# Performance work log

Hardware: AMD Instinct MI355X
Metric: run time of the kernel (lower is better)

## Reference

```python
import jax, jax.numpy as jnp
import numpy as np

N = 100000   # nodes
E = 800000   # edges
F_IN = 16
H = 64       # hidden_dim
L = 4        # num_layers
CD = 8       # contrastive_dim
BN_EPS = 1e-5


def setup_inputs() -> dict:
    key = jax.random.key(0)
    ks = jax.random.split(key, 20)
    s = 0.05
    return {
        "x": jax.random.normal(ks[0], (N, F_IN), jnp.float32),
        "edge_index": jax.random.randint(ks[1], (2, E), 0, N, jnp.int64),
        "batch": jnp.zeros((N,), jnp.int64),
        "enc_w1": jax.random.normal(ks[2], (F_IN, H), jnp.float32) * s,
        "enc_b1": jnp.zeros((H,), jnp.float32),
        "enc_w2": jax.random.normal(ks[3], (H, H), jnp.float32) * s,
        "enc_b2": jnp.zeros((H,), jnp.float32),
        "conv_w": jax.random.normal(ks[4], (L, 2 * H, H), jnp.float32) * s,
        "conv_b": jnp.zeros((L, H), jnp.float32),
        "bn_gamma": jnp.ones((L, H), jnp.float32),
        "bn_beta": jnp.zeros((L, H), jnp.float32),
        "out_w1": jax.random.normal(ks[5], (H, 64), jnp.float32) * s,
        "out_b1": jnp.zeros((64,), jnp.float32),
        "out_w2": jax.random.normal(ks[6], (64, 32), jnp.float32) * s,
        "out_b2": jnp.zeros((32,), jnp.float32),
        "out_w3": jax.random.normal(ks[7], (32, CD), jnp.float32) * s,
        "out_b3": jnp.zeros((CD,), jnp.float32),
    }


def _forward(x, edge_index, enc_w1, enc_b1, enc_w2, enc_b2,
             conv_w, conv_b, bn_gamma, bn_beta,
             out_w1, out_b1, out_w2, out_b2, out_w3, out_b3):
    row, col = edge_index[0], edge_index[1]
    # lc_encode: Linear+ELU, Linear+ELU
    h = jax.nn.elu(x @ enc_w1 + enc_b1)
    feats = jax.nn.elu(h @ enc_w2 + enc_b2)  # (N, H)

    ones = jnp.ones((E, 1), feats.dtype)
    counts = jnp.clip(jax.ops.segment_sum(ones, row, num_segments=N), 1.0)  # (N,1)
    bn_scale = 1.0 / jnp.sqrt(1.0 + BN_EPS)  # eval-mode BN: running_mean=0, running_var=1

    for i in range(L):
        xc = feats[row]               # gather centers (E, H)
        xn = feats[col]               # gather neighbors (E, H)
        ef = jnp.concatenate([xc, xn - xc], axis=-1)      # (E, 2H)
        e = jax.nn.elu(ef @ conv_w[i] + conv_b[i])        # Linear + ELU
        e = (e * bn_scale) * bn_gamma[i] + bn_beta[i]     # BatchNorm (eval); Dropout is identity
        agg = jax.ops.segment_sum(e, row, num_segments=N) / counts
        feats = agg + feats  # residual in Net.forward

    # output head (Dropout identity in eval)
    o = jax.nn.elu(feats @ out_w1 + out_b1)
    o = jax.nn.elu(o @ out_w2 + out_b2)
    return o @ out_w3 + out_b3  # (N, CD)


def reference(x, edge_index, batch, enc_w1, enc_b1, enc_w2, enc_b2,
              conv_w, conv_b, bn_gamma, bn_beta,
              out_w1, out_b1, out_w2, out_b2, out_w3, out_b3):
    out = _forward(x, edge_index, enc_w1, enc_b1, enc_w2, enc_b2,
                   conv_w, conv_b, bn_gamma, bn_beta,
                   out_w1, out_b1, out_w2, out_b2, out_w3, out_b3)
    return (out, batch)
```

## Files before the change

kernel.cpp:

```cpp
#include <hip/hip_runtime.h>

#define NN 100000
#define NE 800000
#define FIN 16
#define H 64
#define NL 4
#define CDIM 8
#define NT 1563
#define NABF 1563
#define NGB 6250
#define NGF 12500
#define ROWS_PER_OWN 12500
#define ECHUNK 2048
#define NCHUNK ((NE + ECHUNK - 1) / ECHUNK)
#define NSC (NCHUNK * 8)
#define CAP 32
#define HOT 8
#define SPILL (CAP - HOT)

typedef __attribute__((ext_vector_type(8))) short bf16x8;
typedef __attribute__((ext_vector_type(4))) float f32x4;

__device__ __forceinline__ float elu(float x) { return x > 0.f ? x : __expf(x) - 1.f; }
__device__ __forceinline__ float4 elu4(float4 v) {
    return make_float4(elu(v.x), elu(v.y), elu(v.z), elu(v.w));
}

__device__ __forceinline__ unsigned short f2bf(float x) {
    union { float f; unsigned int u; } v; v.f = x;
    unsigned int r = v.u + 0x7fffu + ((v.u >> 16) & 1u);
    return (unsigned short)(r >> 16);
}
__device__ __forceinline__ float u2f(unsigned int u) {
    union { unsigned int u; float f; } v; v.u = u;
    return v.f;
}

__global__ __launch_bounds__(256) void k_enc(const float* __restrict__ x,
                                             const float* __restrict__ w1,
                                             const float* __restrict__ b1,
                                             const float* __restrict__ w2,
                                             const float* __restrict__ b2,
                                             float* __restrict__ feats,
                                             int* __restrict__ cnt,
                                             const float* __restrict__ convw,
                                             unsigned short* __restrict__ WT) {
    int tid = threadIdx.x;
    if (blockIdx.x >= NT) {
        int t = (blockIdx.x - NT) * 256 + tid;
        int i = t >> 11;
        int rem = t & 2047;
        int j = rem >> 4;
        int kg = rem & 15;
        const float* W = convw + (size_t)i * 2 * H * H;
        float v[4];
#pragma unroll
        for (int q = 0; q < 4; q++) {
            int k = kg * 4 + q;
            if (j < 64) v[q] = W[k * 64 + j] - W[(64 + k) * 64 + j];
            else        v[q] = W[(64 + k) * 64 + (j - 64)];
        }
        ushort4 p;
        p.x = f2bf(v[0]); p.y = f2bf(v[1]); p.z = f2bf(v[2]); p.w = f2bf(v[3]);
        *(ushort4*)&WT[(size_t)i * 8192 + j * 64 + kg * 4] = p;
        return;
    }
    __shared__ __align__(16) float xs[64 * 16];
    __shared__ __align__(16) float w1s[16 * 64];
    __shared__ __align__(16) float ws[64 * 64];
    __shared__ __align__(16) float fs[64 * 68];
    int base = blockIdx.x * 64;
    {
        int gid = blockIdx.x * 256 + tid;
        if (gid < NN) cnt[gid] = 0;
    }
    {
        size_t ei = (size_t)base * FIN + tid * 4;
        size_t emax = (size_t)NN * FIN - 4;
        if (ei > emax) ei = emax;
        *(float4*)&xs[tid * 4] = *(const float4*)&x[ei];
    }
    ((float4*)w1s)[tid] = ((const float4*)w1)[tid];
#pragma unroll
    for (int r = 0; r < 4; r++) ((float4*)ws)[tid + 256 * r] = ((const float4*)w2)[tid + 256 * r];
    __syncthreads();

    int wave = tid >> 6, j = tid & 63;
    float bb1 = b1[j];
    for (int i = 0; i < 16; i++) {
        int nl = i * 4 + wave;
        float acc = bb1;
#pragma unroll
        for (int k = 0; k < FIN; k++) acc += xs[nl * FIN + k] * w1s[k * 64 + j];
        fs[nl * 68 + j] = elu(acc);
    }
    __syncthreads();

    int cg = tid & 15, ng = tid >> 4;
    int c0 = cg * 4;
    float4 bb = ((const float4*)b2)[cg];
    float4 acc[4];
    acc[0] = bb; acc[1] = bb; acc[2] = bb; acc[3] = bb;
#pragma unroll 2
    for (int kq = 0; kq < 16; kq++) {
        int k0 = kq * 4;
        float4 w0 = *(const float4*)&ws[(k0 + 0) * 64 + c0];
        float4 w1v = *(const float4*)&ws[(k0 + 1) * 64 + c0];
        float4 w2v = *(const float4*)&ws[(k0 + 2) * 64 + c0];
        float4 w3v = *(const float4*)&ws[(k0 + 3) * 64 + c0];
#pragma unroll
        for (int m = 0; m < 4; m++) {
            float4 f = *(const float4*)&fs[(ng * 4 + m) * 68 + k0];
            acc[m].x += f.x * w0.x + f.y * w1v.x + f.z * w2v.x + f.w * w3v.x;
            acc[m].y += f.x * w0.y + f.y * w1v.y + f.z * w2v.y + f.w * w3v.y;
            acc[m].z += f.x * w0.z + f.y * w1v.z + f.z * w2v.z + f.w * w3v.z;
            acc[m].w += f.x * w0.w + f.y * w1v.w + f.z * w2v.w + f.w * w3v.w;
        }
    }
#pragma unroll
    for (int m = 0; m < 4; m++) {
        int n = base + ng * 4 + m;
        if (n < NN) *(float4*)&feats[(size_t)n * 64 + c0] = elu4(acc[m]);
    }
}

__global__ __launch_bounds__(256, 8) void k_scab(const int* __restrict__ row,
                                                 const int* __restrict__ col,
                                                 int* cnt, int* __restrict__ hot,
                                                 int* __restrict__ spill,
                                                 const float* __restrict__ feats,
                                                 const unsigned short* __restrict__ WT,
                                                 const float* __restrict__ convb,
                                                 unsigned short* __restrict__ Am,
                                                 unsigned short* __restrict__ Bm) {
    int tid = threadIdx.x;
    if (blockIdx.x >= NABF) {
        int owner = blockIdx.x & 7;
        int chunk = (blockIdx.x - NABF) >> 3;
        int lo = owner * ROWS_PER_OWN, hi = lo + ROWS_PER_OWN;
        int base = chunk * ECHUNK;
        int end = base + ECHUNK; if (end > NE) end = NE;
        for (int e = base + tid; e < end; e += 256) {
            int r = row[e];
            if (r >= lo && r < hi) {
                int p = atomicAdd(&cnt[r], 1);
                if (p < HOT) hot[(size_t)r * HOT + p] = col[e];
                else if (p < CAP) spill[(size_t)r * SPILL + (p - HOT)] = col[e];
            }
        }
        return;
    }
    int bid = blockIdx.x;
    int wave = tid >> 6, lane = tid & 63;
    int lr = lane & 15, lk = lane >> 4;
    int nb = bid * 64 + wave * 16;
    int n = nb + lr;
    int nc = n < NN ? n : NN - 1;

    bf16x8 ff0, ff1;
    {
        float4 f0 = *(const float4*)&feats[(size_t)nc * 64 + lk * 8];
        float4 f1 = *(const float4*)&feats[(size_t)nc * 64 + lk * 8 + 4];
        float4 f2 = *(const float4*)&feats[(size_t)nc * 64 + 32 + lk * 8];
        float4 f3 = *(const float4*)&feats[(size_t)nc * 64 + 32 + lk * 8 + 4];
        ff0[0] = (short)f2bf(f0.x); ff0[1] = (short)f2bf(f0.y);
        ff0[2] = (short)f2bf(f0.z); ff0[3] = (short)f2bf(f0.w);
        ff0[4] = (short)f2bf(f1.x); ff0[5] = (short)f2bf(f1.y);
        ff0[6] = (short)f2bf(f1.z); ff0[7] = (short)f2bf(f1.w);
        ff1[0] = (short)f2bf(f2.x); ff1[1] = (short)f2bf(f2.y);
        ff1[2] = (short)f2bf(f2.z); ff1[3] = (short)f2bf(f2.w);
        ff1[4] = (short)f2bf(f3.x); ff1[5] = (short)f2bf(f3.y);
        ff1[6] = (short)f2bf(f3.z); ff1[7] = (short)f2bf(f3.w);
    }
#pragma unroll 1
    for (int ct = 0; ct < 8; ct++) {
        bf16x8 w0 = *(const bf16x8*)&WT[(ct * 16 + lr) * 64 + lk * 8];
        bf16x8 w1 = *(const bf16x8*)&WT[(ct * 16 + lr) * 64 + 32 + lk * 8];
        f32x4 acc;
        if (ct < 4) {
            float4 bq = *(const float4*)&convb[ct * 16 + lk * 4];
            acc[0] = bq.x; acc[1] = bq.y; acc[2] = bq.z; acc[3] = bq.w;
        } else {
            acc = (f32x4)(0.0f);
        }
        acc = __builtin_amdgcn_mfma_f32_16x16x32_bf16(w0, ff0, acc, 0, 0, 0);
        acc = __builtin_amdgcn_mfma_f32_16x16x32_bf16(w1, ff1, acc, 0, 0, 0);
        if (n < NN) {
            unsigned short* dst = (ct < 4) ? Am : Bm;
            int wc = (ct & 3) * 16 + lk * 4;
            ushort4 p;
            p.x = f2bf(acc[0]); p.y = f2bf(acc[1]);
            p.z = f2bf(acc[2]); p.w = f2bf(acc[3]);
            *(ushort4*)&dst[(size_t)n * 64 + wc] = p;
        }
    }
}

__global__ __launch_bounds__(256) void k_gab(const unsigned short* __restrict__ Brd,
                                             unsigned short* __restrict__ Am,
                                             unsigned short* __restrict__ Bwr,
                                             const int* __restrict__ cnt,
                                             const int* __restrict__ hot,
                                             const int* __restrict__ spill,
                                             const float* __restrict__ gamma,
                                             const float* __restrict__ beta,
                                             float* __restrict__ feats,
                                             const unsigned short* __restrict__ WT,
                                             const float* __restrict__ convb) {
    __shared__ __align__(16) unsigned short nlds[16 * 72];
    int tid = threadIdx.x;
    int wave = tid >> 6, lane = tid & 63;
    int half = lane >> 5, l = lane & 31;
    int g = l >> 3;
    int cq = l & 7, c0 = cq * 8;
    int nb16 = blockIdx.x * 16;

    const float bs = 0.99999500003749968750f;
    float4 gm0 = *(const float4*)&gamma[c0];
    float4 gm1 = *(const float4*)&gamma[c0 + 4];
    float4 bt0 = *(const float4*)&beta[c0];
    float4 bt1 = *(const float4*)&beta[c0 + 4];

#pragma unroll
    for (int t = 0; t < 2; t++) {
        int j = t * 8 + wave * 2 + half;
        int n = nb16 + j;
        int deg = cnt[n];
        if (deg > CAP) deg = CAP;
        int mycol = (l < HOT) ? hot[(size_t)n * HOT + l]
                              : spill[(size_t)n * SPILL + (l - HOT)];
        uint4 rawA = *(const uint4*)&Am[(size_t)n * H + c0];
        float4 a0 = make_float4(u2f(rawA.x << 16), u2f(rawA.x & 0xffff0000u),
                                u2f(rawA.y << 16), u2f(rawA.y & 0xffff0000u));
        float4 a1 = make_float4(u2f(rawA.z << 16), u2f(rawA.z & 0xffff0000u),
                                u2f(rawA.w << 16), u2f(rawA.w & 0xffff0000u));
        float4 f0, f1;
        if (g == 0) {
            f0 = *(const float4*)&feats[(size_t)n * H + c0];
            f1 = *(const float4*)&feats[(size_t)n * H + c0 + 4];
        }
        float4 acc0 = make_float4(0.f, 0.f, 0.f, 0.f);
        float4 acc1 = make_float4(0.f, 0.f, 0.f, 0.f);
        for (int p0 = 0; p0 < deg; p0 += 4) {
            int p = p0 + g;
            bool valid = p < deg;
            int pc = valid ? p : (deg - 1);
            int c = __shfl(mycol, (half << 5) + pc);
            uint4 raw = *(const uint4*)&Brd[(size_t)c * H + c0];
            float4 b0 = make_float4(u2f(raw.x << 16), u2f(raw.x & 0xffff0000u),
                                    u2f(raw.y << 16), u2f(raw.y & 0xffff0000u));
            float4 b1 = make_float4(u2f(raw.z << 16), u2f(raw.z & 0xffff0000u),
                                    u2f(raw.w << 16), u2f(raw.w & 0xffff0000u));
            float4 v0 = elu4(make_float4(a0.x + b0.x, a0.y + b0.y, a0.z + b0.z, a0.w + b0.w));
            float4 v1 = elu4(make_float4(a1.x + b1.x, a1.y + b1.y, a1.z + b1.z, a1.w + b1.w));
            if (valid) {
                acc0.x += v0.x; acc0.y += v0.y; acc0.z += v0.z; acc0.w += v0.w;
                acc1.x += v1.x; acc1.y += v1.y; acc1.z += v1.z; acc1.w += v1.w;
            }
        }
#pragma unroll
        for (int d = 8; d < 32; d <<= 1) {
            acc0.x += __shfl_xor(acc0.x, d); acc0.y += __shfl_xor(acc0.y, d);
            acc0.z += __shfl_xor(acc0.z, d); acc0.w += __shfl_xor(acc0.w, d);
            acc1.x += __shfl_xor(acc1.x, d); acc1.y += __shfl_xor(acc1.y, d);
            acc1.z += __shfl_xor(acc1.z, d); acc1.w += __shfl_xor(acc1.w, d);
        }
        if (g == 0) {
            if (deg > 0) {
                float inv = bs / (float)deg;
                f0.x += acc0.x * gm0.x * inv + bt0.x;
                f0.y += acc0.y * gm0.y * inv + bt0.y;
                f0.z += acc0.z * gm0.z * inv + bt0.z;
                f0.w += acc0.w * gm0.w * inv + bt0.w;
                f1.x += acc1.x * gm1.x * inv + bt1.x;
                f1.y += acc1.y * gm1.y * inv + bt1.y;
                f1.z += acc1.z * gm1.z * inv + bt1.z;
                f1.w += acc1.w * gm1.w * inv + bt1.w;
                *(float4*)&feats[(size_t)n * H + c0] = f0;
                *(float4*)&feats[(size_t)n * H + c0 + 4] = f1;
            }
            ushort4 pa, pb;
            pa.x = f2bf(f0.x); pa.y = f2bf(f0.y); pa.z = f2bf(f0.z); pa.w = f2bf(f0.w);
            pb.x = f2bf(f1.x); pb.y = f2bf(f1.y); pb.z = f2bf(f1.z); pb.w = f2bf(f1.w);
            *(ushort4*)&nlds[j * 72 + cq * 8] = pa;
            *(ushort4*)&nlds[j * 72 + cq * 8 + 4] = pb;
        }
    }
    __syncthreads();

    {
        int lr = lane & 15, lk = lane >> 4;
        bf16x8 ff[2];
#pragma unroll
        for (int kt = 0; kt < 2; kt++)
            ff[kt] = *(const bf16x8*)&nlds[lr * 72 + kt * 32 + lk * 8];
#pragma unroll
        for (int ctl = 0; ctl < 2; ctl++) {
            int ct = wave * 2 + ctl;
            bf16x8 w0 = *(const bf16x8*)&WT[(ct * 16 + lr) * 64 + lk * 8];
            bf16x8 w1 = *(const bf16x8*)&WT[(ct * 16 + lr) * 64 + 32 + lk * 8];
            f32x4 acc;
            if (ct < 4) {
                float4 bq = *(const float4*)&convb[ct * 16 + lk * 4];
                acc[0] = bq.x; acc[1] = bq.y; acc[2] = bq.z; acc[3] = bq.w;
            } else {
                acc = (f32x4)(0.0f);
            }
            acc = __builtin_amdgcn_mfma_f32_16x16x32_bf16(w0, ff[0], acc, 0, 0, 0);
            acc = __builtin_amdgcn_mfma_f32_16x16x32_bf16(w1, ff[1], acc, 0, 0, 0);
            int n = nb16 + lr;
            unsigned short* dst = (ct < 4) ? Am : Bwr;
            int wc = (ct & 3) * 16 + lk * 4;
            ushort4 p;
            p.x = f2bf(acc[0]); p.y = f2bf(acc[1]);
            p.z = f2bf(acc[2]); p.w = f2bf(acc[3]);
            *(ushort4*)&dst[(size_t)n * 64 + wc] = p;
        }
    }
}

__global__ __launch_bounds__(256) void k_gather(const unsigned short* __restrict__ Am,
                                                const unsigned short* __restrict__ Bm,
                                                const int* __restrict__ cnt,
                                                const int* __restrict__ hot,
                                                const int* __restrict__ spill,
                                                const float* __restrict__ gamma,
                                                const float* __restrict__ beta,
                                                float* __restrict__ feats) {
    int tid = threadIdx.x;
    int wave = tid >> 6, lane = tid & 63;
    int half = lane >> 5, l = lane & 31;
    int n = blockIdx.x * 8 + wave * 2 + half;
    int g = l >> 3;
    int cq = l & 7, c0 = cq * 8;
    int deg = cnt[n];
    if (deg > CAP) deg = CAP;
    int mycol = (l < HOT) ? hot[(size_t)n * HOT + l]
                          : spill[(size_t)n * SPILL + (l - HOT)];
    uint4 rawA = *(const uint4*)&Am[(size_t)n * H + c0];
    float4 a0 = make_float4(u2f(rawA.x << 16), u2f(rawA.x & 0xffff0000u),
                            u2f(rawA.y << 16), u2f(rawA.y & 0xffff0000u));
    float4 a1 = make_float4(u2f(rawA.z << 16), u2f(rawA.z & 0xffff0000u),
                            u2f(rawA.w << 16), u2f(rawA.w & 0xffff0000u));
    float4 f0, f1;
    if (g == 0) {
        f0 = *(const float4*)&feats[(size_t)n * H + c0];
        f1 = *(const float4*)&feats[(size_t)n * H + c0 + 4];
    }
    float4 acc0 = make_float4(0.f, 0.f, 0.f, 0.f);
    float4 acc1 = make_float4(0.f, 0.f, 0.f, 0.f);
    for (int p0 = 0; p0 < deg; p0 += 4) {
        int p = p0 + g;
        bool valid = p < deg;
        int pc = valid ? p : (deg - 1);
        int c = __shfl(mycol, (half << 5) + pc);
        uint4 raw = *(const uint4*)&Bm[(size_t)c * H + c0];
        float4 b0 = make_float4(u2f(raw.x << 16), u2f(raw.x & 0xffff0000u),
                                u2f(raw.y << 16), u2f(raw.y & 0xffff0000u));
        float4 b1 = make_float4(u2f(raw.z << 16), u2f(raw.z & 0xffff0000u),
                                u2f(raw.w << 16), u2f(raw.w & 0xffff0000u));
        float4 v0 = elu4(make_float4(a0.x + b0.x, a0.y + b0.y, a0.z + b0.z, a0.w + b0.w));
        float4 v1 = elu4(make_float4(a1.x + b1.x, a1.y + b1.y, a1.z + b1.z, a1.w + b1.w));
        if (valid) {
            acc0.x += v0.x; acc0.y += v0.y; acc0.z += v0.z; acc0.w += v0.w;
            acc1.x += v1.x; acc1.y += v1.y; acc1.z += v1.z; acc1.w += v1.w;
        }
    }
#pragma unroll
    for (int d = 8; d < 32; d <<= 1) {
        acc0.x += __shfl_xor(acc0.x, d); acc0.y += __shfl_xor(acc0.y, d);
        acc0.z += __shfl_xor(acc0.z, d); acc0.w += __shfl_xor(acc0.w, d);
        acc1.x += __shfl_xor(acc1.x, d); acc1.y += __shfl_xor(acc1.y, d);
        acc1.z += __shfl_xor(acc1.z, d); acc1.w += __shfl_xor(acc1.w, d);
    }
    if (g == 0 && deg > 0) {
        const float bs = 0.99999500003749968750f;
        float inv = bs / (float)deg;
        float4 gm0 = *(const float4*)&gamma[c0];
        float4 gm1 = *(const float4*)&gamma[c0 + 4];
        float4 bt0 = *(const float4*)&beta[c0];
        float4 bt1 = *(const float4*)&beta[c0 + 4];
        f0.x += acc0.x * gm0.x * inv + bt0.x;
        f0.y += acc0.y * gm0.y * inv + bt0.y;
        f0.z += acc0.z * gm0.z * inv + bt0.z;
        f0.w += acc0.w * gm0.w * inv + bt0.w;
        f1.x += acc1.x * gm1.x * inv + bt1.x;
        f1.y += acc1.y * gm1.y * inv + bt1.y;
        f1.z += acc1.z * gm1.z * inv + bt1.z;
        f1.w += acc1.w * gm1.w * inv + bt1.w;
        *(float4*)&feats[(size_t)n * H + c0] = f0;
        *(float4*)&feats[(size_t)n * H + c0 + 4] = f1;
    }
}

__global__ __launch_bounds__(256) void k_head(const float* __restrict__ feats,
                                              const float* __restrict__ w1,
                                              const float* __restrict__ b1,
                                              const float* __restrict__ w2,
                                              const float* __restrict__ b2,
                                              const float* __restrict__ w3,
                                              const float* __restrict__ b3,
                                              const int* __restrict__ batch,
                                              float* __restrict__ out,
                                              float* __restrict__ out2) {
    __shared__ __align__(16) float fs[64 * 68];
    __shared__ __align__(16) float w1s[64 * 64];
    __shared__ __align__(16) float o1s[64 * 68];
    __shared__ __align__(16) float w2s[64 * 32];
    __shared__ __align__(16) float w3s[32 * 8];
    int tid = threadIdx.x;
    int base = blockIdx.x * 64;
#pragma unroll
    for (int r = 0; r < 4; r++) {
        int idx = tid + 256 * r;
        ((float4*)w1s)[idx] = ((const float4*)w1)[idx];
        int rw = idx >> 4, cc = idx & 15;
        int n = base + rw; if (n >= NN) n = NN - 1;
        *(float4*)&fs[rw * 68 + cc * 4] = *(const float4*)&feats[(size_t)n * 64 + cc * 4];
    }
    ((float4*)w2s)[tid] = ((const float4*)w2)[tid];
    ((float4*)w2s)[tid + 256] = ((const float4*)w2)[tid + 256];
    if (tid < 64) ((float4*)w3s)[tid] = ((const float4*)w3)[tid];
    if (tid < 64) {
        int n = base + tid;
        if (n < NN) out2[n] = (float)batch[n];
    }
    __syncthreads();

    int cg = tid & 15, ng = tid >> 4;
    int c0 = cg * 4;
    {
        float4 bb = ((const float4*)b1)[cg];
        float4 acc[4];
        acc[0] = bb; acc[1] = bb; acc[2] = bb; acc[3] = bb;
#pragma unroll 2
        for (int kq = 0; kq < 16; kq++) {
            int k0 = kq * 4;
            float4 w0 = *(const float4*)&w1s[(k0 + 0) * 64 + c0];
            float4 w1v = *(const float4*)&w1s[(k0 + 1) * 64 + c0];
            float4 w2v = *(const float4*)&w1s[(k0 + 2) * 64 + c0];
            float4 w3v = *(const float4*)&w1s[(k0 + 3) * 64 + c0];
#pragma unroll
            for (int m = 0; m < 4; m++) {
                float4 f = *(const float4*)&fs[(ng * 4 + m) * 68 + k0];
                acc[m].x += f.x * w0.x + f.y * w1v.x + f.z * w2v.x + f.w * w3v.x;
                acc[m].y += f.x * w0.y + f.y * w1v.y + f.z * w2v.y + f.w * w3v.y;
                acc[m].z += f.x * w0.z + f.y * w1v.z + f.z * w2v.z + f.w * w3v.z;
                acc[m].w += f.x * w0.w + f.y * w1v.w + f.z * w2v.w + f.w * w3v.w;
            }
        }
        __syncthreads();
#pragma unroll
        for (int m = 0; m < 4; m++)
            *(float4*)&o1s[(ng * 4 + m) * 68 + c0] = elu4(acc[m]);
    }
    __syncthreads();

    float* o2s = fs;
    {
        int cg2 = tid & 7, ng2 = tid >> 3;
        int c20 = cg2 * 4;
        float4 bb = ((const float4*)b2)[cg2];
        float4 acc[2];
        acc[0] = bb; acc[1] = bb;
#pragma unroll 2
        for (int kq = 0; kq < 16; kq++) {
            int k0 = kq * 4;
            float4 w0 = *(const float4*)&w2s[(k0 + 0) * 32 + c20];
            float4 w1v = *(const float4*)&w2s[(k0 + 1) * 32 + c20];
            float4 w2v = *(const float4*)&w2s[(k0 + 2) * 32 + c20];
            float4 w3v = *(const float4*)&w2s[(k0 + 3) * 32 + c20];
#pragma unroll
            for (int m = 0; m < 2; m++) {
                float4 f = *(const float4*)&o1s[(ng2 * 2 + m) * 68 + k0];
                acc[m].x += f.x * w0.x + f.y * w1v.x + f.z * w2v.x + f.w * w3v.x;
                acc[m].y += f.x * w0.y + f.y * w1v.y + f.z * w2v.y + f.w * w3v.y;
                acc[m].z += f.x * w0.z + f.y * w1v.z + f.z * w2v.z + f.w * w3v.z;
                acc[m].w += f.x * w0.w + f.y * w1v.w + f.z * w2v.w + f.w * w3v.w;
            }
        }
#pragma unroll
        for (int m = 0; m < 2; m++)
            *(float4*)&o2s[(ng2 * 2 + m) * 40 + c20] = elu4(acc[m]);
    }
    __syncthreads();

    if (tid < 128) {
        int n3 = tid >> 1, c30 = (tid & 1) * 4;
        float4 acc = ((const float4*)b3)[tid & 1];
#pragma unroll 2
        for (int kq = 0; kq < 8; kq++) {
            int k0 = kq * 4;
            float4 w0 = *(const float4*)&w3s[(k0 + 0) * 8 + c30];
            float4 w1v = *(const float4*)&w3s[(k0 + 1) * 8 + c30];
            float4 w2v = *(const float4*)&w3s[(k0 + 2) * 8 + c30];
            float4 w3v = *(const float4*)&w3s[(k0 + 3) * 8 + c30];
            float4 f = *(const float4*)&o2s[n3 * 40 + k0];
            acc.x += f.x * w0.x + f.y * w1v.x + f.z * w2v.x + f.w * w3v.x;
            acc.y += f.x * w0.y + f.y * w1v.y + f.z * w2v.y + f.w * w3v.y;
            acc.z += f.x * w0.z + f.y * w1v.z + f.z * w2v.z + f.w * w3v.z;
            acc.w += f.x * w0.w + f.y * w1v.w + f.z * w2v.w + f.w * w3v.w;
        }
        int n = base + n3;
        if (n < NN) *(float4*)&out[(size_t)n * 8 + c30] = acc;
    }
}

extern "C" void kernel_launch(void* const* d_in, const int* in_sizes, int n_in,
                              void* d_out, int out_size, void* d_ws, size_t ws_size,
                              hipStream_t stream) {
    const float* x = (const float*)d_in[0];
    const int* edge_index = (const int*)d_in[1];
    const int* batch = (const int*)d_in[2];
    const float* enc_w1 = (const float*)d_in[3];
    const float* enc_b1 = (const float*)d_in[4];
    const float* enc_w2 = (const float*)d_in[5];
    const float* enc_b2 = (const float*)d_in[6];
    const float* conv_w = (const float*)d_in[7];
    const float* conv_b = (const float*)d_in[8];
    const float* bn_gamma = (const float*)d_in[9];
    const float* bn_beta = (const float*)d_in[10];
    const float* out_w1 = (const float*)d_in[11];
    const float* out_b1 = (const float*)d_in[12];
    const float* out_w2 = (const float*)d_in[13];
    const float* out_b2 = (const float*)d_in[14];
    const float* out_w3 = (const float*)d_in[15];
    const float* out_b3 = (const float*)d_in[16];

    const int* row = edge_index;
    const int* col = edge_index + NE;

    float* feats = (float*)d_ws;
    unsigned short* Abuf = (unsigned short*)(feats + (size_t)NN * H);
    unsigned short* Bbuf0 = Abuf + (size_t)NN * H;
    unsigned short* Bbuf1 = Bbuf0 + (size_t)NN * H;
    int* cnt = (int*)(Bbuf1 + (size_t)NN * H);
    int* hot = cnt + NN;
    int* spill = hot + (size_t)NN * HOT;
    unsigned short* WT = (unsigned short*)(spill + (size_t)NN * SPILL);

    float* out = (float*)d_out;

    k_enc<<<NT + 32, 256, 0, stream>>>(x, enc_w1, enc_b1, enc_w2, enc_b2, feats, cnt,
                                       conv_w, WT);
    k_scab<<<NABF + NSC, 256, 0, stream>>>(row, col, cnt, hot, spill,
                                           feats, WT, conv_b, Abuf, Bbuf0);

    unsigned short* Brd = Bbuf0;
    unsigned short* Bwr = Bbuf1;
    for (int i = 0; i < NL - 1; i++) {
        k_gab<<<NGB, 256, 0, stream>>>(Brd, Abuf, Bwr, cnt, hot, spill,
                                       bn_gamma + (size_t)i * H, bn_beta + (size_t)i * H,
                                       feats, WT + (size_t)(i + 1) * 8192,
                                       conv_b + (size_t)(i + 1) * H);
        unsigned short* tmp = Brd; Brd = Bwr; Bwr = tmp;
    }
    k_gather<<<NGF, 256, 0, stream>>>(Abuf, Brd, cnt, hot, spill,
                                      bn_gamma + (size_t)(NL - 1) * H,
                                      bn_beta + (size_t)(NL - 1) * H, feats);

    k_head<<<NT, 256, 0, stream>>>(feats, out_w1, out_b1, out_w2, out_b2,
                                   out_w3, out_b3, batch, out,
                                   out + (size_t)NN * CDIM);
}
```

Before: 369.6 us.

## Fuse final gather-aggregate layer with output MLP head into one kernel

Merges the last-layer neighbor gather/aggregation kernel with the three-layer output head, so each 8-node block aggregates its features into shared memory and immediately runs the MLP. This removes the final feats write/read round trip and one kernel launch. The cost is that each of the 12500 blocks now reloads about 25 KB of head weights into shared memory, and the head matmuls now use a less register-blocked scalar scheme over only 8 nodes.

After: 388.1 us. 1.05x slower.

```diff
diff --git a/kernel.cpp b/kernel.cpp
--- a/kernel.cpp
+++ b/kernel.cpp
@@ -9,7 +9,7 @@
 #define NT 1563
 #define NABF 1563
 #define NGB 6250
-#define NGF 12500
+#define NGH 12500
 #define ROWS_PER_OWN 12500
 #define ECHUNK 2048
 #define NCHUNK ((NE + ECHUNK - 1) / ECHUNK)
@@ -319,190 +319,140 @@
     }
 }
 
-__global__ __launch_bounds__(256) void k_gather(const unsigned short* __restrict__ Am,
-                                                const unsigned short* __restrict__ Bm,
-                                                const int* __restrict__ cnt,
-                                                const int* __restrict__ hot,
-                                                const int* __restrict__ spill,
-                                                const float* __restrict__ gamma,
-                                                const float* __restrict__ beta,
-                                                float* __restrict__ feats) {
-    int tid = threadIdx.x;
-    int wave = tid >> 6, lane = tid & 63;
-    int half = lane >> 5, l = lane & 31;
-    int n = blockIdx.x * 8 + wave * 2 + half;
-    int g = l >> 3;
-    int cq = l & 7, c0 = cq * 8;
-    int deg = cnt[n];
-    if (deg > CAP) deg = CAP;
-    int mycol = (l < HOT) ? hot[(size_t)n * HOT + l]
-                          : spill[(size_t)n * SPILL + (l - HOT)];
-    uint4 rawA = *(const uint4*)&Am[(size_t)n * H + c0];
-    float4 a0 = make_float4(u2f(rawA.x << 16), u2f(rawA.x & 0xffff0000u),
-                            u2f(rawA.y << 16), u2f(rawA.y & 0xffff0000u));
-    float4 a1 = make_float4(u2f(rawA.z << 16), u2f(rawA.z & 0xffff0000u),
-                            u2f(rawA.w << 16), u2f(rawA.w & 0xffff0000u));
-    float4 f0, f1;
-    if (g == 0) {
-        f0 = *(const float4*)&feats[(size_t)n * H + c0];
-        f1 = *(const float4*)&feats[(size_t)n * H + c0 + 4];
-    }
-    float4 acc0 = make_float4(0.f, 0.f, 0.f, 0.f);
-    float4 acc1 = make_float4(0.f, 0.f, 0.f, 0.f);
-    for (int p0 = 0; p0 < deg; p0 += 4) {
-        int p = p0 + g;
-        bool valid = p < deg;
-        int pc = valid ? p : (deg - 1);
-        int c = __shfl(mycol, (half << 5) + pc);
-        uint4 raw = *(const uint4*)&Bm[(size_t)c * H + c0];
-        float4 b0 = make_float4(u2f(raw.x << 16), u2f(raw.x & 0xffff0000u),
-                                u2f(raw.y << 16), u2f(raw.y & 0xffff0000u));
-        float4 b1 = make_float4(u2f(raw.z << 16), u2f(raw.z & 0xffff0000u),
-                                u2f(raw.w << 16), u2f(raw.w & 0xffff0000u));
-        float4 v0 = elu4(make_float4(a0.x + b0.x, a0.y + b0.y, a0.z + b0.z, a0.w + b0.w));
-        float4 v1 = elu4(make_float4(a1.x + b1.x, a1.y + b1.y, a1.z + b1.z, a1.w + b1.w));
-        if (valid) {
-            acc0.x += v0.x; acc0.y += v0.y; acc0.z += v0.z; acc0.w += v0.w;
-            acc1.x += v1.x; acc1.y += v1.y; acc1.z += v1.z; acc1.w += v1.w;
-        }
-    }
-#pragma unroll
-    for (int d = 8; d < 32; d <<= 1) {
-        acc0.x += __shfl_xor(acc0.x, d); acc0.y += __shfl_xor(acc0.y, d);
-        acc0.z += __shfl_xor(acc0.z, d); acc0.w += __shfl_xor(acc0.w, d);
-        acc1.x += __shfl_xor(acc1.x, d); acc1.y += __shfl_xor(acc1.y, d);
-        acc1.z += __shfl_xor(acc1.z, d); acc1.w += __shfl_xor(acc1.w, d);
-    }
-    if (g == 0 && deg > 0) {
-        const float bs = 0.99999500003749968750f;
-        float inv = bs / (float)deg;
-        float4 gm0 = *(const float4*)&gamma[c0];
-        float4 gm1 = *(const float4*)&gamma[c0 + 4];
-        float4 bt0 = *(const float4*)&beta[c0];
-        float4 bt1 = *(const float4*)&beta[c0 + 4];
-        f0.x += acc0.x * gm0.x * inv + bt0.x;
-        f0.y += acc0.y * gm0.y * inv + bt0.y;
-        f0.z += acc0.z * gm0.z * inv + bt0.z;
-        f0.w += acc0.w * gm0.w * inv + bt0.w;
-        f1.x += acc1.x * gm1.x * inv + bt1.x;
-        f1.y += acc1.y * gm1.y * inv + bt1.y;
-        f1.z += acc1.z * gm1.z * inv + bt1.z;
-        f1.w += acc1.w * gm1.w * inv + bt1.w;
-        *(float4*)&feats[(size_t)n * H + c0] = f0;
-        *(float4*)&feats[(size_t)n * H + c0 + 4] = f1;
-    }
-}
-
-__global__ __launch_bounds__(256) void k_head(const float* __restrict__ feats,
-                                              const float* __restrict__ w1,
-                                              const float* __restrict__ b1,
-                                              const float* __restrict__ w2,
-                                              const float* __restrict__ b2,
-                                              const float* __restrict__ w3,
-                                              const float* __restrict__ b3,
-                                              const int* __restrict__ batch,
-                                              float* __restrict__ out,
-                                              float* __restrict__ out2) {
-    __shared__ __align__(16) float fs[64 * 68];
+__global__ __launch_bounds__(256) void k_ghead(const unsigned short* __restrict__ Am,
+                                               const unsigned short* __restrict__ Bm,
+                                               const int* __restrict__ cnt,
+                                               const int* __restrict__ hot,
+                                               const int* __restrict__ spill,
+                                               const float* __restrict__ gamma,
+                                               const float* __restrict__ beta,
+                                               const float* __restrict__ feats,
+                                               const float* __restrict__ w1,
+                                               const float* __restrict__ b1,
+                                               const float* __restrict__ w2,
+                                               const float* __restrict__ b2,
+                                               const float* __restrict__ w3,
+                                               const float* __restrict__ b3,
+                                               const int* __restrict__ batch,
+                                               float* __restrict__ out,
+                                               float* __restrict__ out2) {
     __shared__ __align__(16) float w1s[64 * 64];
-    __shared__ __align__(16) float o1s[64 * 68];
     __shared__ __align__(16) float w2s[64 * 32];
     __shared__ __align__(16) float w3s[32 * 8];
+    __shared__ __align__(16) float fs[8 * 68];
+    __shared__ __align__(16) float o1s[8 * 68];
     int tid = threadIdx.x;
-    int base = blockIdx.x * 64;
-#pragma unroll
-    for (int r = 0; r < 4; r++) {
-        int idx = tid + 256 * r;
-        ((float4*)w1s)[idx] = ((const float4*)w1)[idx];
-        int rw = idx >> 4, cc = idx & 15;
-        int n = base + rw; if (n >= NN) n = NN - 1;
-        *(float4*)&fs[rw * 68 + cc * 4] = *(const float4*)&feats[(size_t)n * 64 + cc * 4];
-    }
+    int base8 = blockIdx.x * 8;
+
+#pragma unroll
+    for (int r = 0; r < 4; r++) ((float4*)w1s)[tid + 256 * r] = ((const float4*)w1)[tid + 256 * r];
     ((float4*)w2s)[tid] = ((const float4*)w2)[tid];
     ((float4*)w2s)[tid + 256] = ((const float4*)w2)[tid + 256];
     if (tid < 64) ((float4*)w3s)[tid] = ((const float4*)w3)[tid];
+    if (tid < 8) out2[base8 + tid] = (float)batch[base8 + tid];
+
+    {
+        int wave = tid >> 6, lane = tid & 63;
+        int half = lane >> 5, l = lane & 31;
+        int j8 = wave * 2 + half;
+        int n = base8 + j8;
+        int g = l >> 3;
+        int cq = l & 7, c0 = cq * 8;
+        int deg = cnt[n];
+        if (deg > CAP) deg = CAP;
+        int mycol = (l < HOT) ? hot[(size_t)n * HOT + l]
+                              : spill[(size_t)n * SPILL + (l - HOT)];
+        uint4 rawA = *(const uint4*)&Am[(size_t)n * H + c0];
+        float4 a0 = make_float4(u2f(rawA.x << 16), u2f(rawA.x & 0xffff0000u),
+                                u2f(rawA.y << 16), u2f(rawA.y & 0xffff0000u));
+        float4 a1 = make_float4(u2f(rawA.z << 16), u2f(rawA.z & 0xffff0000u),
+                                u2f(rawA.w << 16), u2f(rawA.w & 0xffff0000u));
+        float4 f0, f1;
+        if (g == 0) {
+            f0 = *(const float4*)&feats[(size_t)n * H + c0];
+            f1 = *(const float4*)&feats[(size_t)n * H + c0 + 4];
+        }
+        float4 acc0 = make_float4(0.f, 0.f, 0.f, 0.f);
+        float4 acc1 = make_float4(0.f, 0.f, 0.f, 0.f);
+        for (int p0 = 0; p0 < deg; p0 += 4) {
+            int p = p0 + g;
+            bool valid = p < deg;
+            int pc = valid ? p : (deg - 1);
+            int c = __shfl(mycol, (half << 5) + pc);
+            uint4 raw = *(const uint4*)&Bm[(size_t)c * H + c0];
+            float4 b0 = make_float4(u2f(raw.x << 16), u2f(raw.x & 0xffff0000u),
+                                    u2f(raw.y << 16), u2f(raw.y & 0xffff0000u));
+            float4 b1 = make_float4(u2f(raw.z << 16), u2f(raw.z & 0xffff0000u),
+                                    u2f(raw.w << 16), u2f(raw.w & 0xffff0000u));
+            float4 v0 = elu4(make_float4(a0.x + b0.x, a0.y + b0.y, a0.z + b0.z, a0.w + b0.w));
+            float4 v1 = elu4(make_float4(a1.x + b1.x, a1.y + b1.y, a1.z + b1.z, a1.w + b1.w));
+            if (valid) {
+                acc0.x += v0.x; acc0.y += v0.y; acc0.z += v0.z; acc0.w += v0.w;
+                acc1.x += v1.x; acc1.y += v1.y; acc1.z += v1.z; acc1.w += v1.w;
+            }
+        }
+#pragma unroll
+        for (int d = 8; d < 32; d <<= 1) {
+            acc0.x += __shfl_xor(acc0.x, d); acc0.y += __shfl_xor(acc0.y, d);
+            acc0.z += __shfl_xor(acc0.z, d); acc0.w += __shfl_xor(acc0.w, d);
+            acc1.x += __shfl_xor(acc1.x, d); acc1.y += __shfl_xor(acc1.y, d);
+            acc1.z += __shfl_xor(acc1.z, d); acc1.w += __shfl_xor(acc1.w, d);
+        }
+        if (g == 0) {
+            if (deg > 0) {
+                const float bs = 0.99999500003749968750f;
+                float inv = bs / (float)deg;
+                float4 gm0 = *(const float4*)&gamma[c0];
+                float4 gm1 = *(const float4*)&gamma[c0 + 4];
+                float4 bt0 = *(const float4*)&beta[c0];
+                float4 bt1 = *(const float4*)&beta[c0 + 4];
+                f0.x += acc0.x * gm0.x * inv + bt0.x;
+                f0.y += acc0.y * gm0.y * inv + bt0.y;
+                f0.z += acc0.z * gm0.z * inv + bt0.z;
+                f0.w += acc0.w * gm0.w * inv + bt0.w;
+                f1.x += acc1.x * gm1.x * inv + bt1.x;
+                f1.y += acc1.y * gm1.y * inv + bt1.y;
+                f1.z += acc1.z * gm1.z * inv + bt1.z;
+                f1.w += acc1.w * gm1.w * inv + bt1.w;
+            }
+            *(float4*)&fs[j8 * 68 + c0] = f0;
+            *(float4*)&fs[j8 * 68 + c0 + 4] = f1;
+        }
+    }
+    __syncthreads();
+
+    {
+        int j = tid & 63, w = tid >> 6;
+        float a0 = b1[j], a1 = a0;
+#pragma unroll 4
+        for (int k = 0; k < 64; k++) {
+            float wv = w1s[k * 64 + j];
+            a0 += fs[(2 * w) * 68 + k] * wv;
+            a1 += fs[(2 * w + 1) * 68 + k] * wv;
+        }
+        o1s[(2 * w) * 68 + j] = elu(a0);
+        o1s[(2 * w + 1) * 68 + j] = elu(a1);
+    }
+    __syncthreads();
+
+    float* o2s = fs;
+    {
+        int node = tid >> 5, j2 = tid & 31;
+        float a = b2[j2];
+#pragma unroll 4
+        for (int k = 0; k < 64; k++) a += o1s[node * 68 + k] * w2s[k * 32 + j2];
+        float r = elu(a);
+        __syncthreads();
+        o2s[node * 40 + j2] = r;
+    }
+    __syncthreads();
+
     if (tid < 64) {
-        int n = base + tid;
-        if (n < NN) out2[n] = (float)batch[n];
-    }
-    __syncthreads();
-
-    int cg = tid & 15, ng = tid >> 4;
-    int c0 = cg * 4;
-    {
-        float4 bb = ((const float4*)b1)[cg];
-        float4 acc[4];
-        acc[0] = bb; acc[1] = bb; acc[2] = bb; acc[3] = bb;
-#pragma unroll 2
-        for (int kq = 0; kq < 16; kq++) {
-            int k0 = kq * 4;
-            float4 w0 = *(const float4*)&w1s[(k0 + 0) * 64 + c0];
-            float4 w1v = *(const float4*)&w1s[(k0 + 1) * 64 + c0];
-            float4 w2v = *(const float4*)&w1s[(k0 + 2) * 64 + c0];
-            float4 w3v = *(const float4*)&w1s[(k0 + 3) * 64 + c0];
-#pragma unroll
-            for (int m = 0; m < 4; m++) {
-                float4 f = *(const float4*)&fs[(ng * 4 + m) * 68 + k0];
-                acc[m].x += f.x * w0.x + f.y * w1v.x + f.z * w2v.x + f.w * w3v.x;
-                acc[m].y += f.x * w0.y + f.y * w1v.y + f.z * w2v.y + f.w * w3v.y;
-                acc[m].z += f.x * w0.z + f.y * w1v.z + f.z * w2v.z + f.w * w3v.z;
-                acc[m].w += f.x * w0.w + f.y * w1v.w + f.z * w2v.w + f.w * w3v.w;
-            }
-        }
-        __syncthreads();
-#pragma unroll
-        for (int m = 0; m < 4; m++)
-            *(float4*)&o1s[(ng * 4 + m) * 68 + c0] = elu4(acc[m]);
-    }
-    __syncthreads();
-
-    float* o2s = fs;
-    {
-        int cg2 = tid & 7, ng2 = tid >> 3;
-        int c20 = cg2 * 4;
-        float4 bb = ((const float4*)b2)[cg2];
-        float4 acc[2];
-        acc[0] = bb; acc[1] = bb;
-#pragma unroll 2
-        for (int kq = 0; kq < 16; kq++) {
-            int k0 = kq * 4;
-            float4 w0 = *(const float4*)&w2s[(k0 + 0) * 32 + c20];
-            float4 w1v = *(const float4*)&w2s[(k0 + 1) * 32 + c20];
-            float4 w2v = *(const float4*)&w2s[(k0 + 2) * 32 + c20];
-            float4 w3v = *(const float4*)&w2s[(k0 + 3) * 32 + c20];
-#pragma unroll
-            for (int m = 0; m < 2; m++) {
-                float4 f = *(const float4*)&o1s[(ng2 * 2 + m) * 68 + k0];
-                acc[m].x += f.x * w0.x + f.y * w1v.x + f.z * w2v.x + f.w * w3v.x;
-                acc[m].y += f.x * w0.y + f.y * w1v.y + f.z * w2v.y + f.w * w3v.y;
-                acc[m].z += f.x * w0.z + f.y * w1v.z + f.z * w2v.z + f.w * w3v.z;
-                acc[m].w += f.x * w0.w + f.y * w1v.w + f.z * w2v.w + f.w * w3v.w;
-            }
-        }
-#pragma unroll
-        for (int m = 0; m < 2; m++)
-            *(float4*)&o2s[(ng2 * 2 + m) * 40 + c20] = elu4(acc[m]);
-    }
-    __syncthreads();
-
-    if (tid < 128) {
-        int n3 = tid >> 1, c30 = (tid & 1) * 4;
-        float4 acc = ((const float4*)b3)[tid & 1];
-#pragma unroll 2
-        for (int kq = 0; kq < 8; kq++) {
-            int k0 = kq * 4;
-            float4 w0 = *(const float4*)&w3s[(k0 + 0) * 8 + c30];
-            float4 w1v = *(const float4*)&w3s[(k0 + 1) * 8 + c30];
-            float4 w2v = *(const float4*)&w3s[(k0 + 2) * 8 + c30];
-            float4 w3v = *(const float4*)&w3s[(k0 + 3) * 8 + c30];
-            float4 f = *(const float4*)&o2s[n3 * 40 + k0];
-            acc.x += f.x * w0.x + f.y * w1v.x + f.z * w2v.x + f.w * w3v.x;
-            acc.y += f.x * w0.y + f.y * w1v.y + f.z * w2v.y + f.w * w3v.y;
-            acc.z += f.x * w0.z + f.y * w1v.z + f.z * w2v.z + f.w * w3v.z;
-            acc.w += f.x * w0.w + f.y * w1v.w + f.z * w2v.w + f.w * w3v.w;
-        }
-        int n = base + n3;
-        if (n < NN) *(float4*)&out[(size_t)n * 8 + c30] = acc;
+        int node = tid >> 3, c3 = tid & 7;
+        float a = b3[c3];
+#pragma unroll 4
+        for (int k = 0; k < 32; k++) a += o2s[node * 40 + k] * w3s[k * 8 + c3];
+        out[(size_t)(base8 + node) * 8 + c3] = a;
     }
 }
 
@@ -555,11 +505,9 @@
                                        conv_b + (size_t)(i + 1) * H);
         unsigned short* tmp = Brd; Brd = Bwr; Bwr = tmp;
     }
-    k_gather<<<NGF, 256, 0, stream>>>(Abuf, Brd, cnt, hot, spill,
-                                      bn_gamma + (size_t)(NL - 1) * H,
-                                      bn_beta + (size_t)(NL - 1) * H, feats);
-
-    k_head<<<NT, 256, 0, stream>>>(feats, out_w1, out_b1, out_w2, out_b2,
-                                   out_w3, out_b3, batch, out,
-                                   out + (size_t)NN * CDIM);
-}
+    k_ghead<<<NGH, 256, 0, stream>>>(Abuf, Brd, cnt, hot, spill,
+                                     bn_gamma + (size_t)(NL - 1) * H,
+                                     bn_beta + (size_t)(NL - 1) * H, feats,
+                                     out_w1, out_b1, out_w2, out_b2, out_w3, out_b3,
+                                     batch, out, out + (size_t)NN * CDIM);
+}
```

## Fuse layer kernels into persistent cooperative kernel with grid sync and atomic tile tickets

Applied to the files above, without the earlier changes.

The three per-layer gather/MFMA kernels and the final gather kernel are replaced by one persistent cooperative kernel. It loops over the layers with grid.sync between them and takes 16-node tiles from an atomic ticket counter that k_enc zeroes each call. The aim is to remove kernel launch gaps and tail effects between layers. In exchange it adds per-tile atomic and barrier overhead, caps residency at the occupancy limit, and grid-wide barriers can cost as much as launch boundaries.

Result: slower. 1.424 ms (+285.3%).

```diff
diff --git a/kernel.cpp b/kernel.cpp
--- a/kernel.cpp
+++ b/kernel.cpp
@@ -1,4 +1,7 @@
 #include <hip/hip_runtime.h>
+#include <hip/hip_cooperative_groups.h>
+
+namespace cg = cooperative_groups;
 
 #define NN 100000
 #define NE 800000
@@ -44,7 +47,8 @@
                                              float* __restrict__ feats,
                                              int* __restrict__ cnt,
                                              const float* __restrict__ convw,
-                                             unsigned short* __restrict__ WT) {
+                                             unsigned short* __restrict__ WT,
+                                             int* __restrict__ tickets) {
     int tid = threadIdx.x;
     if (blockIdx.x >= NT) {
         int t = (blockIdx.x - NT) * 256 + tid;
@@ -74,6 +78,7 @@
         int gid = blockIdx.x * 256 + tid;
         if (gid < NN) cnt[gid] = 0;
     }
+    if (blockIdx.x == 0 && tid < 4) tickets[tid] = 0;
     {
         size_t ei = (size_t)base * FIN + tid * 4;
         size_t emax = (size_t)NN * FIN - 4;
@@ -96,9 +101,9 @@
     }
     __syncthreads();
 
-    int cg = tid & 15, ng = tid >> 4;
-    int c0 = cg * 4;
-    float4 bb = ((const float4*)b2)[cg];
+    int cg_ = tid & 15, ng = tid >> 4;
+    int c0 = cg_ * 4;
+    float4 bb = ((const float4*)b2)[cg_];
     float4 acc[4];
     acc[0] = bb; acc[1] = bb; acc[2] = bb; acc[3] = bb;
 #pragma unroll 2
@@ -196,24 +201,25 @@
     }
 }
 
-__global__ __launch_bounds__(256) void k_gab(const unsigned short* __restrict__ Brd,
-                                             unsigned short* __restrict__ Am,
-                                             unsigned short* __restrict__ Bwr,
-                                             const int* __restrict__ cnt,
-                                             const int* __restrict__ hot,
-                                             const int* __restrict__ spill,
-                                             const float* __restrict__ gamma,
-                                             const float* __restrict__ beta,
-                                             float* __restrict__ feats,
-                                             const unsigned short* __restrict__ WT,
-                                             const float* __restrict__ convb) {
-    __shared__ __align__(16) unsigned short nlds[16 * 72];
+__device__ __forceinline__ void gab_tile(int tile,
+                                         const unsigned short* __restrict__ Brd,
+                                         unsigned short* __restrict__ Am,
+                                         unsigned short* __restrict__ Bwr,
+                                         const int* __restrict__ cnt,
+                                         const int* __restrict__ hot,
+                                         const int* __restrict__ spill,
+                                         const float* __restrict__ gamma,
+                                         const float* __restrict__ beta,
+                                         float* __restrict__ feats,
+                                         const unsigned short* __restrict__ WT,
+                                         const float* __restrict__ convb,
+                                         unsigned short* nlds) {
     int tid = threadIdx.x;
     int wave = tid >> 6, lane = tid & 63;
     int half = lane >> 5, l = lane & 31;
     int g = l >> 3;
     int cq = l & 7, c0 = cq * 8;
-    int nb16 = blockIdx.x * 16;
+    int nb16 = tile * 16;
 
     const float bs = 0.99999500003749968750f;
     float4 gm0 = *(const float4*)&gamma[c0];
@@ -319,18 +325,19 @@
     }
 }
 
-__global__ __launch_bounds__(256) void k_gather(const unsigned short* __restrict__ Am,
-                                                const unsigned short* __restrict__ Bm,
-                                                const int* __restrict__ cnt,
-                                                const int* __restrict__ hot,
-                                                const int* __restrict__ spill,
-                                                const float* __restrict__ gamma,
-                                                const float* __restrict__ beta,
-                                                float* __restrict__ feats) {
+__device__ __forceinline__ void g3_tile(int tile,
+                                        const unsigned short* __restrict__ Am,
+                                        const unsigned short* __restrict__ Bm,
+                                        const int* __restrict__ cnt,
+                                        const int* __restrict__ hot,
+                                        const int* __restrict__ spill,
+                                        const float* __restrict__ gamma,
+                                        const float* __restrict__ beta,
+                                        float* __restrict__ feats) {
     int tid = threadIdx.x;
     int wave = tid >> 6, lane = tid & 63;
     int half = lane >> 5, l = lane & 31;
-    int n = blockIdx.x * 8 + wave * 2 + half;
+    int n = tile * 8 + wave * 2 + half;
     int g = l >> 3;
     int cq = l & 7, c0 = cq * 8;
     int deg = cnt[n];
@@ -393,6 +400,81 @@
     }
 }
 
+__global__ __launch_bounds__(256) void k_gab(const unsigned short* __restrict__ Brd,
+                                             unsigned short* __restrict__ Am,
+                                             unsigned short* __restrict__ Bwr,
+                                             const int* __restrict__ cnt,
+                                             const int* __restrict__ hot,
+                                             const int* __restrict__ spill,
+                                             const float* __restrict__ gamma,
+                                             const float* __restrict__ beta,
+                                             float* __restrict__ feats,
+                                             const unsigned short* __restrict__ WT,
+                                             const float* __restrict__ convb) {
+    __shared__ __align__(16) unsigned short nlds[16 * 72];
+    gab_tile(blockIdx.x, Brd, Am, Bwr, cnt, hot, spill, gamma, beta, feats, WT, convb, nlds);
+}
+
+__global__ __launch_bounds__(256) void k_gather(const unsigned short* __restrict__ Am,
+                                                const unsigned short* __restrict__ Bm,
+                                                const int* __restrict__ cnt,
+                                                const int* __restrict__ hot,
+                                                const int* __restrict__ spill,
+                                                const float* __restrict__ gamma,
+                                                const float* __restrict__ beta,
+                                                float* __restrict__ feats) {
+    g3_tile(blockIdx.x, Am, Bm, cnt, hot, spill, gamma, beta, feats);
+}
+
+__global__ __launch_bounds__(256, 8) void k_mega(unsigned short* Am,
+                                                 unsigned short* Bbuf0,
+                                                 unsigned short* Bbuf1,
+                                                 const int* cnt,
+                                                 const int* hot,
+                                                 const int* spill,
+                                                 const float* bn_gamma,
+                                                 const float* bn_beta,
+                                                 float* feats,
+                                                 const unsigned short* WT,
+                                                 const float* convb,
+                                                 int* tickets) {
+    cg::grid_group grid = cg::this_grid();
+    __shared__ __align__(16) unsigned short nlds[16 * 72];
+    __shared__ int s_tile;
+    int tid = threadIdx.x;
+
+    for (int layer = 0; layer < 3; layer++) {
+        const unsigned short* Brd = (layer & 1) ? Bbuf1 : Bbuf0;
+        unsigned short* Bwr = (layer & 1) ? Bbuf0 : Bbuf1;
+        const float* gamma = bn_gamma + (size_t)layer * H;
+        const float* beta = bn_beta + (size_t)layer * H;
+        const unsigned short* WTl = WT + (size_t)(layer + 1) * 8192;
+        const float* cb = convb + (size_t)(layer + 1) * H;
+        while (true) {
+            __syncthreads();
+            if (tid == 0) s_tile = atomicAdd(&tickets[layer], 1);
+            __syncthreads();
+            int t = s_tile;
+            if (t >= NGB) break;
+            gab_tile(t, Brd, Am, Bwr, cnt, hot, spill, gamma, beta, feats, WTl, cb, nlds);
+        }
+        __threadfence();
+        grid.sync();
+    }
+    {
+        const float* gamma = bn_gamma + (size_t)3 * H;
+        const float* beta = bn_beta + (size_t)3 * H;
+        while (true) {
+            __syncthreads();
+            if (tid == 0) s_tile = atomicAdd(&tickets[3], 1);
+            __syncthreads();
+            int t = s_tile;
+            if (t >= NGF) break;
+            g3_tile(t, Am, Bbuf1, cnt, hot, spill, gamma, beta, feats);
+        }
+    }
+}
+
 __global__ __launch_bounds__(256) void k_head(const float* __restrict__ feats,
                                               const float* __restrict__ w1,
                                               const float* __restrict__ b1,
@@ -427,10 +509,10 @@
     }
     __syncthreads();
 
-    int cg = tid & 15, ng = tid >> 4;
-    int c0 = cg * 4;
+    int cg_ = tid & 15, ng = tid >> 4;
+    int c0 = cg_ * 4;
     {
-        float4 bb = ((const float4*)b1)[cg];
+        float4 bb = ((const float4*)b1)[cg_];
         float4 acc[4];
         acc[0] = bb; acc[1] = bb; acc[2] = bb; acc[3] = bb;
 #pragma unroll 2
@@ -538,26 +620,45 @@
     int* hot = cnt + NN;
     int* spill = hot + (size_t)NN * HOT;
     unsigned short* WT = (unsigned short*)(spill + (size_t)NN * SPILL);
+    int* tickets = (int*)(WT + 4 * 8192);
 
     float* out = (float*)d_out;
 
     k_enc<<<NT + 32, 256, 0, stream>>>(x, enc_w1, enc_b1, enc_w2, enc_b2, feats, cnt,
-                                       conv_w, WT);
+                                       conv_w, WT, tickets);
     k_scab<<<NABF + NSC, 256, 0, stream>>>(row, col, cnt, hot, spill,
                                            feats, WT, conv_b, Abuf, Bbuf0);
 
-    unsigned short* Brd = Bbuf0;
-    unsigned short* Bwr = Bbuf1;
-    for (int i = 0; i < NL - 1; i++) {
-        k_gab<<<NGB, 256, 0, stream>>>(Brd, Abuf, Bwr, cnt, hot, spill,
-                                       bn_gamma + (size_t)i * H, bn_beta + (size_t)i * H,
-                                       feats, WT + (size_t)(i + 1) * 8192,
-                                       conv_b + (size_t)(i + 1) * H);
-        unsigned short* tmp = Brd; Brd = Bwr; Bwr = tmp;
-    }
-    k_gather<<<NGF, 256, 0, stream>>>(Abuf, Brd, cnt, hot, spill,
-                                      bn_gamma + (size_t)(NL - 1) * H,
-                                      bn_beta + (size_t)(NL - 1) * H, feats);
+    int blocksPerCU = 0;
+    hipError_t oerr = hipOccupancyMaxActiveBlocksPerMultiprocessor(&blocksPerCU, k_mega, 256, 0);
+    if (oerr != hipSuccess || blocksPerCU < 1) blocksPerCU = 4;
+    int grid = blocksPerCU * 256;
+    if (grid > 2048) grid = 2048;
+
+    unsigned short* Am_a = Abuf;
+    const int* cnt_c = cnt;
+    const int* hot_c = hot;
+    const int* spill_c = spill;
+    const unsigned short* WT_c = WT;
+    void* margs[] = {&Am_a, &Bbuf0, &Bbuf1, (void*)&cnt_c, (void*)&hot_c, (void*)&spill_c,
+                     (void*)&bn_gamma, (void*)&bn_beta, &feats, (void*)&WT_c,
+                     (void*)&conv_b, &tickets};
+    hipError_t cerr = hipLaunchCooperativeKernel((const void*)k_mega, dim3(grid), dim3(256),
+                                                 margs, 0, stream);
+    if (cerr != hipSuccess) {
+        unsigned short* Brd = Bbuf0;
+        unsigned short* Bwr = Bbuf1;
+        for (int i = 0; i < NL - 1; i++) {
+            k_gab<<<NGB, 256, 0, stream>>>(Brd, Abuf, Bwr, cnt, hot, spill,
+                                           bn_gamma + (size_t)i * H, bn_beta + (size_t)i * H,
+                                           feats, WT + (size_t)(i + 1) * 8192,
+                                           conv_b + (size_t)(i + 1) * H);
+            unsigned short* tmp = Brd; Brd = Bwr; Bwr = tmp;
+        }
+        k_gather<<<NGF, 256, 0, stream>>>(Abuf, Brd, cnt, hot, spill,
+                                          bn_gamma + (size_t)(NL - 1) * H,
+                                          bn_beta + (size_t)(NL - 1) * H, feats);
+    }
 
     k_head<<<NT, 256, 0, stream>>>(feats, out_w1, out_b1, out_w2, out_b2,
                                    out_w3, out_b3, batch, out,
```
